# Performance work log

Measured on AMD Instinct MI355X. Metric: run time of the kernel, lower is better.

The kernel has to match this reference:

```python
import jax, jax.numpy as jnp
import numpy as np

EPS = 1e-12

def _l2norm(x):
    # F.normalize(p=2, dim=-1) semantics: x / max(||x||, eps)
    n = jnp.sqrt(jnp.sum(x * x, axis=-1, keepdims=True))
    return x / jnp.maximum(n, EPS)

def _split_heads(x, h):
    b, l, d = x.shape
    return x.reshape(b, l, h, d // h).transpose(0, 2, 1, 3)  # (B,H,L,dh)

def _join_heads(x):
    b, h, l, dh = x.shape
    return x.transpose(0, 2, 1, 3).reshape(b, l, h * dh)

def setup_inputs() -> dict:
    key = jax.random.key(0)
    B, L, D = 4, 4096, 1024
    ks = jax.random.split(key, 12)
    s = 1.0 / np.sqrt(D)
    inp = {
        "queries": jax.random.normal(ks[0], (B, L, D), jnp.float32),
        "values": jax.random.normal(ks[1], (B, L, D), jnp.float32),
        "keys": jax.random.normal(ks[2], (B, L, D), jnp.float32),
        "key_attention_mask": jnp.ones((B, L), jnp.float32),
        "Wq": jax.random.uniform(ks[3], (D, D), jnp.float32, -s, s),
        "bq": jax.random.uniform(ks[4], (D,), jnp.float32, -s, s),
        "Wk": jax.random.uniform(ks[5], (D, D), jnp.float32, -s, s),
        "bk": jax.random.uniform(ks[6], (D,), jnp.float32, -s, s),
        "Wv": jax.random.uniform(ks[7], (D, D), jnp.float32, -s, s),
        "bv": jax.random.uniform(ks[8], (D,), jnp.float32, -s, s),
        "Wo": jax.random.uniform(ks[9], (D, D), jnp.float32, -s, s),
        "bo": jax.random.uniform(ks[10], (D,), jnp.float32, -s, s),
    }
    return inp

def reference(queries, values, keys, key_attention_mask, Wq, bq, Wk, bk, Wv, bv, Wo, bo):
    nhead = 16
    L2 = keys.shape[1]
    qp = jnp.einsum('bld,ed->ble', queries, Wq) + bq
    kp = jnp.einsum('bld,ed->ble', keys, Wk) + bk
    vp = jnp.einsum('bld,ed->ble', values, Wv) + bv
    Q = _split_heads(qp, nhead)   # (B,H,L1,dh)
    K = _split_heads(kp, nhead)   # (B,H,L2,dh)
    V = _split_heads(vp, nhead)   # (B,H,L2,dh)
    V_minus = jnp.minimum(V, 0.0)
    V_plus = jnp.maximum(V, 0.0)
    Q = jax.nn.sigmoid(Q)
    scaled_K = jax.nn.sigmoid(K) / L2
    # AmplitudeEmbedding: L2-normalize feature maps along feature dim
    Q = _l2norm(Q)
    scaled_K = _l2norm(scaled_K)
    kv_plus = jnp.einsum('bhld,bhlc,bl->bhdc', scaled_K, V_plus, key_attention_mask)
    heads_plus = _l2norm(jnp.einsum('bhld,bhdc->bhlc', Q, kv_plus))
    kv_minus = jnp.einsum('bhld,bhlc,bl->bhdc', scaled_K, V_minus, key_attention_mask)
    heads_minus = _l2norm(jnp.einsum('bhld,bhdc->bhlc', Q, kv_minus))
    out = _join_heads(heads_plus + heads_minus)  # (B,L1,D)
    return jnp.einsum('blc,dc->bld', out, Wo) + bo
```

## Files before the change

### kernel.cpp

```cpp
#include <hip/hip_runtime.h>
#include <stdint.h>

#define B_  4
#define L_  4096
#define D_  1024
#define H_  16
#define DH  64
#define M_  (B_*L_)

typedef _Float16 f16;
typedef __attribute__((ext_vector_type(8))) _Float16 f16x8;
typedef __attribute__((ext_vector_type(4))) _Float16 f16x4;
typedef __attribute__((ext_vector_type(4))) float    f32x4;

__device__ __forceinline__ void cp16(const void* g, void* l) {
  __builtin_amdgcn_global_load_lds(
      (const __attribute__((address_space(1))) void*)g,
      (__attribute__((address_space(3))) void*)l,
      16, 0, 0);
}

__global__ __launch_bounds__(256) void k_cvt_f16(const float* __restrict__ x,
                                                 f16* __restrict__ y, int n8) {
  int i = blockIdx.x * 256 + threadIdx.x;
  if (i >= n8) return;
  const float4* xv = (const float4*)x;
  float4 a = xv[2*i], b = xv[2*i+1];
  f16x8 o;
  o[0]=(f16)a.x; o[1]=(f16)a.y; o[2]=(f16)a.z; o[3]=(f16)a.w;
  o[4]=(f16)b.x; o[5]=(f16)b.y; o[6]=(f16)b.z; o[7]=(f16)b.w;
  ((f16x8*)y)[i] = o;
}

__global__ __launch_bounds__(256) void k_split_w(const float* __restrict__ x,
                                                 f16* __restrict__ hi,
                                                 f16* __restrict__ lo, int n4) {
  int i = blockIdx.x * 256 + threadIdx.x;
  if (i >= n4) return;
  float4 a = ((const float4*)x)[i];
  f16 h0=(f16)a.x, h1=(f16)a.y, h2=(f16)a.z, h3=(f16)a.w;
  f16x4 hv = {h0, h1, h2, h3};
  f16x4 lv = {(f16)(a.x-(float)h0), (f16)(a.y-(float)h1),
              (f16)(a.z-(float)h2), (f16)(a.w-(float)h3)};
  ((f16x4*)hi)[i] = hv;
  ((f16x4*)lo)[i] = lv;
}

__global__ __launch_bounds__(256) void k_gemm_hi(
    const f16* __restrict__ A, const f16* __restrict__ Bh,
    const float* __restrict__ bias, const float* __restrict__ mask,
    float* __restrict__ Cf, f16* __restrict__ Ch, int mode,
    int M, int N, int K) {
  __shared__ __align__(16) f16 sA[128*32];
  __shared__ __align__(16) f16 sB[128*32];
  const int t = threadIdx.x;
  const int nbn = N >> 7;
  const int bm = (blockIdx.x / nbn) << 7;
  const int bn = (blockIdx.x % nbn) << 7;
  const int lane = t & 63, wave = t >> 6;
  const int wm = (wave & 1) << 6, wn = (wave >> 1) << 6;
  const int rowA = t >> 2;
  const int cc   = (t & 3) << 3;

  const f16* Ag  = A  + (size_t)(bm + rowA) * K + cc;
  const f16* Ag2 = Ag + (size_t)64 * K;
  const f16* Bg  = Bh + (size_t)(bn + rowA) * K + cc;
  const f16* Bg2 = Bg + (size_t)64 * K;
  f16* lA  = &sA[t * 8];  f16* lA2 = &sA[(t + 256) * 8];
  f16* lB  = &sB[t * 8];  f16* lB2 = &sB[(t + 256) * 8];

  f32x4 acc[4][4] = {};
  const int fm = lane & 15;
  const int fk = (lane >> 4) << 3;

  for (int k0 = 0; k0 < K; k0 += 32) {
    __syncthreads();
    cp16(Ag + k0, lA);  cp16(Ag2 + k0, lA2);
    cp16(Bg + k0, lB);  cp16(Bg2 + k0, lB2);
    __syncthreads();
    f16x8 af[4], bf[4];
#pragma unroll
    for (int i = 0; i < 4; ++i) {
      af[i] = *(const f16x8*)&sA[(wm + i*16 + fm) * 32 + fk];
      bf[i] = *(const f16x8*)&sB[(wn + i*16 + fm) * 32 + fk];
    }
#pragma unroll
    for (int i = 0; i < 4; ++i)
#pragma unroll
      for (int j = 0; j < 4; ++j)
        acc[i][j] = __builtin_amdgcn_mfma_f32_16x16x32_f16(af[i], bf[j], acc[i][j], 0, 0, 0);
  }
  const int cr   = (lane >> 4) << 2;
  const int ccol = lane & 15;
  if (mode == 0) {
#pragma unroll
    for (int j = 0; j < 4; ++j) {
      int gn = bn + wn + j*16 + ccol;
      float bv = bias[gn];
#pragma unroll
      for (int i = 0; i < 4; ++i) {
        float* Cp = Cf + (size_t)(bm + wm + i*16 + cr) * N + gn;
#pragma unroll
        for (int r = 0; r < 4; ++r) Cp[(size_t)r * N] = acc[i][j][r] + bv;
      }
    }
  } else {
    float bvj[4];
#pragma unroll
    for (int j = 0; j < 4; ++j) bvj[j] = bias[bn + wn + j*16 + ccol];
#pragma unroll
    for (int i = 0; i < 4; ++i)
#pragma unroll
      for (int r = 0; r < 4; ++r) {
        int gm = bm + wm + i*16 + cr + r;
        float s[4], ss = 0.f;
#pragma unroll
        for (int j = 0; j < 4; ++j) {
          float v = acc[i][j][r] + bvj[j];
          s[j] = 1.0f / (1.0f + __expf(-v));
          ss += s[j] * s[j];
        }
        ss += __shfl_xor(ss, 1, 64);
        ss += __shfl_xor(ss, 2, 64);
        ss += __shfl_xor(ss, 4, 64);
        ss += __shfl_xor(ss, 8, 64);
        float sc = 1.0f / fmaxf(sqrtf(ss), 1e-12f);
        if (mask) sc *= mask[gm];
#pragma unroll
        for (int j = 0; j < 4; ++j)
          Ch[(size_t)gm * N + bn + wn + j*16 + ccol] = (f16)(s[j] * sc);
      }
  }
}

__global__ __launch_bounds__(256) void k_gemm_ws(
    const f16* __restrict__ A, const f16* __restrict__ Bhi,
    const f16* __restrict__ Blo, const float* __restrict__ bias,
    float* __restrict__ Cf, f16* __restrict__ Ch, int M, int N, int K) {
  __shared__ __align__(16) f16 sA [128*32];
  __shared__ __align__(16) f16 sBh[128*32];
  __shared__ __align__(16) f16 sBl[128*32];
  const int t = threadIdx.x;
  const int nbn = N >> 7;
  const int bm = (blockIdx.x / nbn) << 7;
  const int bn = (blockIdx.x % nbn) << 7;
  const int lane = t & 63, wave = t >> 6;
  const int wm = (wave & 1) << 6, wn = (wave >> 1) << 6;
  const int rowA = t >> 2;
  const int cc   = (t & 3) << 3;

  const f16* Ag   = A   + (size_t)(bm + rowA) * K + cc;
  const f16* Ag2  = Ag  + (size_t)64 * K;
  const f16* Bgh  = Bhi + (size_t)(bn + rowA) * K + cc;
  const f16* Bgh2 = Bgh + (size_t)64 * K;
  const f16* Bgl  = Blo + (size_t)(bn + rowA) * K + cc;
  const f16* Bgl2 = Bgl + (size_t)64 * K;

  f16* lA   = &sA [t * 8];  f16* lA2  = &sA [(t + 256) * 8];
  f16* lBh  = &sBh[t * 8];  f16* lBh2 = &sBh[(t + 256) * 8];
  f16* lBl  = &sBl[t * 8];  f16* lBl2 = &sBl[(t + 256) * 8];

  f32x4 acc[4][4] = {};
  const int fm = lane & 15;
  const int fk = (lane >> 4) << 3;

  for (int k0 = 0; k0 < K; k0 += 32) {
    __syncthreads();
    cp16(Ag  + k0, lA );  cp16(Ag2  + k0, lA2 );
    cp16(Bgh + k0, lBh);  cp16(Bgh2 + k0, lBh2);
    cp16(Bgl + k0, lBl);  cp16(Bgl2 + k0, lBl2);
    __syncthreads();
    f16x8 af[4], bh[4], bl[4];
#pragma unroll
    for (int i = 0; i < 4; ++i) {
      af[i] = *(const f16x8*)&sA [(wm + i*16 + fm) * 32 + fk];
      bh[i] = *(const f16x8*)&sBh[(wn + i*16 + fm) * 32 + fk];
      bl[i] = *(const f16x8*)&sBl[(wn + i*16 + fm) * 32 + fk];
    }
#pragma unroll
    for (int i = 0; i < 4; ++i)
#pragma unroll
      for (int j = 0; j < 4; ++j) {
        acc[i][j] = __builtin_amdgcn_mfma_f32_16x16x32_f16(af[i], bh[j], acc[i][j], 0, 0, 0);
        acc[i][j] = __builtin_amdgcn_mfma_f32_16x16x32_f16(af[i], bl[j], acc[i][j], 0, 0, 0);
      }
  }
  const int cr   = (lane >> 4) << 2;
  const int ccol = lane & 15;
#pragma unroll
  for (int j = 0; j < 4; ++j) {
    int gn = bn + wn + j*16 + ccol;
    float bv = bias[gn];
#pragma unroll
    for (int i = 0; i < 4; ++i) {
      size_t gm = (size_t)(bm + wm + i*16 + cr);
      if (Ch) {
#pragma unroll
        for (int r = 0; r < 4; ++r)
          Ch[(gm + r) * N + gn] = (f16)(acc[i][j][r] + bv);
      } else {
        float* Cp = Cf + gm * N + gn;
#pragma unroll
        for (int r = 0; r < 4; ++r) Cp[(size_t)r * N] = acc[i][j][r] + bv;
      }
    }
  }
}

#define SKT 72
__global__ __launch_bounds__(256) void k_kv_mfma(const f16* __restrict__ Kh,
                                                 const f16* __restrict__ Vh,
                                                 float* __restrict__ part) {
  __shared__ __align__(16) f16 sKt[64 * SKT];
  __shared__ __align__(16) f16 sVt[128 * SKT];
  int head = blockIdx.x >> 3, chunk = blockIdx.x & 7;
  int b = head >> 4, h = head & 15;
  int t = threadIdx.x, lane = t & 63, wave = t >> 6;
  int lp = t & 31, g8 = (t >> 5) << 3;
  size_t rowbase = (size_t)b * L_ + (size_t)chunk * 512;
  const f16* Kb = Kh + rowbase * D_ + h * DH;
  const f16* Vb = Vh + rowbase * D_ + h * DH;

  const int fm = lane & 15, fk = (lane >> 4) << 3;
  const int wm2 = (wave & 1) * 2;
  const int wn4 = (wave >> 1) * 4;
  f32x4 acc[2][4] = {};

  for (int l0 = 0; l0 < 512; l0 += 64) {
    __syncthreads();
    {
      const f16* r0 = Kb + (size_t)(l0 + 2*lp) * D_ + g8;
      f16x8 a0 = *(const f16x8*)r0;
      f16x8 a1 = *(const f16x8*)(r0 + D_);
#pragma unroll
      for (int j = 0; j < 8; ++j) {
        union { f16 h2[2]; uint32_t u; } pk;
        pk.h2[0] = a0[j]; pk.h2[1] = a1[j];
        *(uint32_t*)&sKt[(g8 + j) * SKT + 2*lp] = pk.u;
      }
      const f16* v0p = Vb + (size_t)(l0 + 2*lp) * D_ + g8;
      f16x8 b0 = *(const f16x8*)v0p;
      f16x8 b1 = *(const f16x8*)(v0p + D_);
#pragma unroll
      for (int j = 0; j < 8; ++j) {
        float x0 = (float)b0[j], x1 = (float)b1[j];
        union { f16 h2[2]; uint32_t u; } pp, pm;
        pp.h2[0] = (f16)fmaxf(x0, 0.f); pp.h2[1] = (f16)fmaxf(x1, 0.f);
        pm.h2[0] = (f16)fminf(x0, 0.f); pm.h2[1] = (f16)fminf(x1, 0.f);
        *(uint32_t*)&sVt[(g8 + j) * SKT + 2*lp]        = pp.u;
        *(uint32_t*)&sVt[(64 + g8 + j) * SKT + 2*lp]   = pm.u;
      }
    }
    __syncthreads();
#pragma unroll
    for (int ks = 0; ks < 2; ++ks) {
      f16x8 af[2], bf[4];
#pragma unroll
      for (int i = 0; i < 2; ++i)
        af[i] = *(const f16x8*)&sKt[((wm2+i)*16 + fm) * SKT + ks*32 + fk];
#pragma unroll
      for (int j = 0; j < 4; ++j)
        bf[j] = *(const f16x8*)&sVt[((wn4+j)*16 + fm) * SKT + ks*32 + fk];
#pragma unroll
      for (int i = 0; i < 2; ++i)
#pragma unroll
        for (int j = 0; j < 4; ++j)
          acc[i][j] = __builtin_amdgcn_mfma_f32_16x16x32_f16(af[i], bf[j], acc[i][j], 0, 0, 0);
    }
  }
  const int cr = (lane >> 4) << 2, ccol = lane & 15;
  float* pb = part + (size_t)(head * 8 + chunk) * 8192;
#pragma unroll
  for (int i = 0; i < 2; ++i)
#pragma unroll
    for (int j = 0; j < 4; ++j) {
      int d = (wm2 + i) * 16 + cr;
      int c2 = (wn4 + j) * 16 + ccol;
#pragma unroll
      for (int r = 0; r < 4; ++r)
        pb[(d + r) * 128 + c2] = acc[i][j][r];
    }
}

__global__ __launch_bounds__(256) void k_kv_reduce(const float* __restrict__ part,
                                                   float* __restrict__ kv) {
  int i = blockIdx.x * 256 + threadIdx.x;
  int head = i >> 13, dc = i & 8191;
  float s = 0.f;
#pragma unroll
  for (int c = 0; c < 8; ++c) s += part[(size_t)(head * 8 + c) * 8192 + dc];
  kv[i] = s;
}

__global__ __launch_bounds__(256) void k_kv_cvt(const float* __restrict__ kvb,
                                                f16* __restrict__ kvh) {
  int head = blockIdx.x, t = threadIdx.x;
  int c = t >> 1, half = t & 1;
  const float* src = kvb + (size_t)head * 8192 + half * 32 * 128 + c;
  f16* dst = kvh + (size_t)head * 8192 + c * 64 + half * 32;
  f16 buf[32];
#pragma unroll
  for (int kk = 0; kk < 32; ++kk) buf[kk] = (f16)src[kk * 128];
#pragma unroll
  for (int q = 0; q < 4; ++q) ((f16x8*)dst)[q] = *(const f16x8*)&buf[q * 8];
}

#define SH 72
__global__ __launch_bounds__(256) void k_heads_mfma(const f16* __restrict__ Qh,
                                                    const f16* __restrict__ kvh,
                                                    f16* __restrict__ O) {
  __shared__ __align__(16) f16 sQ [128 * SH];
  __shared__ __align__(16) f16 sKV[128 * SH];
  int bi = blockIdx.x;
  int head = bi >> 5, mt = bi & 31;
  int b = head >> 4, h = head & 15;
  int t = threadIdx.x, lane = t & 63, wave = t >> 6;
  size_t qbase = ((size_t)(b * L_ + mt * 128)) * D_ + h * DH;
  const f16* kvp = kvh + (size_t)head * 8192;
#pragma unroll
  for (int p = 0; p < 4; ++p) {
    int c = p * 256 + t;
    int row = c >> 3, off = (c & 7) * 8;
    f16x8 q = *(const f16x8*)(Qh + qbase + (size_t)row * D_ + off);
    *(f16x8*)&sQ[row * SH + off] = q;
    f16x8 kv8 = *(const f16x8*)(kvp + row * 64 + off);
    *(f16x8*)&sKV[row * SH + off] = kv8;
  }
  __syncthreads();

  const int fm = lane & 15, fk = (lane >> 4) << 3;
  const int wm = wave * 32;
  f32x4 acc[2][8] = {};
#pragma unroll
  for (int ks = 0; ks < 2; ++ks) {
    f16x8 a0 = *(const f16x8*)&sQ[(wm + fm) * SH + ks * 32 + fk];
    f16x8 a1 = *(const f16x8*)&sQ[(wm + 16 + fm) * SH + ks * 32 + fk];
#pragma unroll
    for (int j = 0; j < 8; ++j) {
      f16x8 bj = *(const f16x8*)&sKV[(j * 16 + fm) * SH + ks * 32 + fk];
      acc[0][j] = __builtin_amdgcn_mfma_f32_16x16x32_f16(a0, bj, acc[0][j], 0, 0, 0);
      acc[1][j] = __builtin_amdgcn_mfma_f32_16x16x32_f16(a1, bj, acc[1][j], 0, 0, 0);
    }
  }
  const int cr = (lane >> 4) << 2, ccol = lane & 15;
#pragma unroll
  for (int i = 0; i < 2; ++i)
#pragma unroll
    for (int r = 0; r < 4; ++r) {
      int row = wm + i * 16 + cr + r;
      float sp = 0.f, sm = 0.f;
#pragma unroll
      for (int j = 0; j < 4; ++j) {
        sp += acc[i][j][r] * acc[i][j][r];
        sm += acc[i][j + 4][r] * acc[i][j + 4][r];
      }
      sp += __shfl_xor(sp, 1, 64); sm += __shfl_xor(sm, 1, 64);
      sp += __shfl_xor(sp, 2, 64); sm += __shfl_xor(sm, 2, 64);
      sp += __shfl_xor(sp, 4, 64); sm += __shfl_xor(sm, 4, 64);
      sp += __shfl_xor(sp, 8, 64); sm += __shfl_xor(sm, 8, 64);
      float rp = 1.0f / fmaxf(sqrtf(sp), 1e-12f);
      float rm = 1.0f / fmaxf(sqrtf(sm), 1e-12f);
#pragma unroll
      for (int j = 0; j < 4; ++j) {
        float o = acc[i][j][r] * rp + acc[i][j + 4][r] * rm;
        O[qbase + (size_t)row * D_ + j * 16 + ccol] = (f16)o;
      }
    }
}

extern "C" void kernel_launch(void* const* d_in, const int* in_sizes, int n_in,
                              void* d_out, int out_size, void* d_ws, size_t ws_size,
                              hipStream_t stream) {
  const float* queries = (const float*)d_in[0];
  const float* values  = (const float*)d_in[1];
  const float* keys    = (const float*)d_in[2];
  const float* mask    = (const float*)d_in[3];
  const float* Wq = (const float*)d_in[4];  const float* bq = (const float*)d_in[5];
  const float* Wk = (const float*)d_in[6];  const float* bk = (const float*)d_in[7];
  const float* Wv = (const float*)d_in[8];  const float* bv = (const float*)d_in[9];
  const float* Wo = (const float*)d_in[10]; const float* bo = (const float*)d_in[11];
  float* out = (float*)d_out;

  const size_t MB = 1024ull * 1024ull;
  const size_t NEED = 160 * MB;
  if (ws_size < NEED) return;

  char* ws = (char*)d_ws;
  const size_t DD = (size_t)D_ * D_;
  f16*   WH   = (f16*)(ws);
  f16*   WL   = (f16*)(ws + 8 * MB);
  f16*   Ah   = (f16*)(ws + 12 * MB);
  f16*   Qh   = (f16*)(ws + 44 * MB);
  float* kvb  = (float*)(ws + 76 * MB);
  f16*   kvh  = (f16*)(ws + 78 * MB);
  float* part = (float*)(ws + 80 * MB);
  f16*   kp   = (f16*)(ws + 96 * MB);
  f16*   vp   = (f16*)(ws + 128 * MB);

  const int DD8 = (int)(DD / 8);
  const int DD4 = (int)(DD / 4);
  k_cvt_f16<<<DD8 / 256, 256, 0, stream>>>(Wq, WH + 0 * DD, DD8);
  k_cvt_f16<<<DD8 / 256, 256, 0, stream>>>(Wk, WH + 1 * DD, DD8);
  k_split_w<<<DD4 / 256, 256, 0, stream>>>(Wv, WH + 2 * DD, WL + 0 * DD, DD4);
  k_split_w<<<DD4 / 256, 256, 0, stream>>>(Wo, WH + 3 * DD, WL + 1 * DD, DD4);

  const int n8 = M_ * D_ / 8;
  const int gGemm = (M_ / 128) * (D_ / 128);

  k_cvt_f16<<<n8 / 256, 256, 0, stream>>>(queries, Ah, n8);
  k_gemm_hi<<<gGemm, 256, 0, stream>>>(Ah, WH + 0 * DD, bq, nullptr, nullptr, Qh, 1, M_, D_, D_);
  k_cvt_f16<<<n8 / 256, 256, 0, stream>>>(keys, Ah, n8);
  k_gemm_hi<<<gGemm, 256, 0, stream>>>(Ah, WH + 1 * DD, bk, mask, nullptr, kp, 1, M_, D_, D_);
  k_cvt_f16<<<n8 / 256, 256, 0, stream>>>(values, Ah, n8);
  k_gemm_ws<<<gGemm, 256, 0, stream>>>(Ah, WH + 2 * DD, WL + 0 * DD, bv, nullptr, vp, M_, D_, D_);

  k_kv_mfma<<<64 * 8, 256, 0, stream>>>(kp, vp, part);
  k_kv_reduce<<<64 * 8192 / 256, 256, 0, stream>>>(part, kvb);
  k_kv_cvt<<<64, 256, 0, stream>>>(kvb, kvh);
  k_heads_mfma<<<64 * 32, 256, 0, stream>>>(Qh, kvh, Ah);

  k_gemm_ws<<<gGemm, 256, 0, stream>>>(Ah, WH + 3 * DD, WL + 1 * DD, bo, out, nullptr, M_, D_, D_);
}
```

Baseline: 615.0 us.

## Replace GEMMs with 256x256 double-buffered 8-wave kernel and interleaved hi/lo weights

Replaces the two 128x128 GEMM kernels with a single 512-thread kernel that uses 256x256 tiles, 64-wide K steps, XOR-swizzled LDS and double-buffered async global-to-LDS loads. MFMA phases are interleaved with loads and use setprio and barriers. The hi/lo split weights are interleaved row-wise into one 2N matrix, so the split-precision GEMMs become plain GEMMs over N=2048 whose paired column tiles are summed in the epilogue. Blocks are also remapped across the 8 XCDs. The aim is more data reuse and better MFMA utilization, at the cost of large LDS usage, register pressure and fragile hand scheduling.

```diff
diff --git a/kernel.cpp b/kernel.cpp
--- a/kernel.cpp
+++ b/kernel.cpp
@@ -19,6 +19,21 @@
       (__attribute__((address_space(3))) void*)l,
       16, 0, 0);
 }
+
+#define MFMA(a,b,c) __builtin_amdgcn_mfma_f32_16x16x32_f16(a,b,c,0,0,0)
+
+#define PH_IN do { __builtin_amdgcn_s_barrier(); \
+  asm volatile("s_waitcnt lgkmcnt(0)" ::: "memory"); \
+  __builtin_amdgcn_sched_barrier(0); \
+  __builtin_amdgcn_s_setprio(1); } while (0)
+#define PH_OUT do { __builtin_amdgcn_s_setprio(0); \
+  __builtin_amdgcn_sched_barrier(0); \
+  asm volatile("" ::: "memory"); \
+  __builtin_amdgcn_s_barrier(); } while (0)
+#define PH_OUT_VM(nimm) do { __builtin_amdgcn_s_setprio(0); \
+  __builtin_amdgcn_sched_barrier(0); \
+  asm volatile("s_waitcnt vmcnt(" #nimm ")" ::: "memory"); \
+  __builtin_amdgcn_s_barrier(); } while (0)
 
 __global__ __launch_bounds__(256) void k_cvt_f16(const float* __restrict__ x,
                                                  f16* __restrict__ y, int n8) {
@@ -33,86 +48,197 @@
 }
 
 __global__ __launch_bounds__(256) void k_split_w(const float* __restrict__ x,
-                                                 f16* __restrict__ hi,
-                                                 f16* __restrict__ lo, int n4) {
+                                                 f16* __restrict__ cat, int n4) {
   int i = blockIdx.x * 256 + threadIdx.x;
   if (i >= n4) return;
   float4 a = ((const float4*)x)[i];
+  int n  = i >> 8;
+  int k4 = i & 255;
   f16 h0=(f16)a.x, h1=(f16)a.y, h2=(f16)a.z, h3=(f16)a.w;
   f16x4 hv = {h0, h1, h2, h3};
   f16x4 lv = {(f16)(a.x-(float)h0), (f16)(a.y-(float)h1),
               (f16)(a.z-(float)h2), (f16)(a.w-(float)h3)};
-  ((f16x4*)hi)[i] = hv;
-  ((f16x4*)lo)[i] = lv;
-}
-
-__global__ __launch_bounds__(256) void k_gemm_hi(
-    const f16* __restrict__ A, const f16* __restrict__ Bh,
+  size_t rh = (size_t)((n >> 4) * 32 + (n & 15));
+  ((f16x4*)cat)[rh * 256 + k4]        = hv;
+  ((f16x4*)cat)[(rh + 16) * 256 + k4] = lv;
+}
+
+__global__ __launch_bounds__(512, 2) void k_gemm8(
+    const f16* __restrict__ A, const f16* __restrict__ Bw,
     const float* __restrict__ bias, const float* __restrict__ mask,
     float* __restrict__ Cf, f16* __restrict__ Ch, int mode,
     int M, int N, int K) {
-  __shared__ __align__(16) f16 sA[128*32];
-  __shared__ __align__(16) f16 sB[128*32];
+  __shared__ __align__(16) char sA[65536];
+  __shared__ __align__(16) char sB[65536];
   const int t = threadIdx.x;
-  const int nbn = N >> 7;
-  const int bm = (blockIdx.x / nbn) << 7;
-  const int bn = (blockIdx.x % nbn) << 7;
+  const int nbn = N >> 8;
+  int bid = blockIdx.x;
+  {
+    int cpx = (int)gridDim.x >> 3;
+    bid = (bid & 7) * cpx + (bid >> 3);
+  }
+  const int bm = (bid / nbn) << 8;
+  const int bn = (bid % nbn) << 8;
   const int lane = t & 63, wave = t >> 6;
-  const int wm = (wave & 1) << 6, wn = (wave >> 1) << 6;
-  const int rowA = t >> 2;
-  const int cc   = (t & 3) << 3;
-
-  const f16* Ag  = A  + (size_t)(bm + rowA) * K + cc;
-  const f16* Ag2 = Ag + (size_t)64 * K;
-  const f16* Bg  = Bh + (size_t)(bn + rowA) * K + cc;
-  const f16* Bg2 = Bg + (size_t)64 * K;
-  f16* lA  = &sA[t * 8];  f16* lA2 = &sA[(t + 256) * 8];
-  f16* lB  = &sB[t * 8];  f16* lB2 = &sB[(t + 256) * 8];
-
-  f32x4 acc[4][4] = {};
-  const int fm = lane & 15;
-  const int fk = (lane >> 4) << 3;
-
-  for (int k0 = 0; k0 < K; k0 += 32) {
-    __syncthreads();
-    cp16(Ag + k0, lA);  cp16(Ag2 + k0, lA2);
-    cp16(Bg + k0, lB);  cp16(Bg2 + k0, lB2);
-    __syncthreads();
-    f16x8 af[4], bf[4];
-#pragma unroll
-    for (int i = 0; i < 4; ++i) {
-      af[i] = *(const f16x8*)&sA[(wm + i*16 + fm) * 32 + fk];
-      bf[i] = *(const f16x8*)&sB[(wn + i*16 + fm) * 32 + fk];
-    }
-#pragma unroll
-    for (int i = 0; i < 4; ++i)
-#pragma unroll
-      for (int j = 0; j < 4; ++j)
-        acc[i][j] = __builtin_amdgcn_mfma_f32_16x16x32_f16(af[i], bf[j], acc[i][j], 0, 0, 0);
-  }
-  const int cr   = (lane >> 4) << 2;
-  const int ccol = lane & 15;
-  if (mode == 0) {
-#pragma unroll
-    for (int j = 0; j < 4; ++j) {
-      int gn = bn + wn + j*16 + ccol;
-      float bv = bias[gn];
-#pragma unroll
-      for (int i = 0; i < 4; ++i) {
-        float* Cp = Cf + (size_t)(bm + wm + i*16 + cr) * N + gn;
-#pragma unroll
-        for (int r = 0; r < 4; ++r) Cp[(size_t)r * N] = acc[i][j][r] + bv;
-      }
-    }
-  } else {
+  const int wm = wave >> 2;
+  const int wn = wave & 3;
+  const int fm = lane & 15, fkb = lane >> 4;
+
+  auto SA_ = [&](int T, int buf, int half) {
+#pragma unroll
+    for (int q = 0; q < 2; ++q) {
+      int li = (q << 9) + t;
+      int row = li >> 3, cb = li & 7;
+      const f16* g = A + (size_t)(bm + (half << 7) + row) * K
+                       + (T << 6) + ((cb ^ (row & 7)) << 3);
+      cp16(g, sA + buf * 32768 + half * 16384 + li * 16);
+    }
+  };
+  auto SB_ = [&](int T, int buf, int half) {
+#pragma unroll
+    for (int q = 0; q < 2; ++q) {
+      int li = (q << 9) + t;
+      int row = li >> 3, cb = li & 7;
+      const f16* g = Bw + (size_t)(bn + (half << 7) + row) * K
+                        + (T << 6) + ((cb ^ (row & 7)) << 3);
+      cp16(g, sB + buf * 32768 + half * 16384 + li * 16);
+    }
+  };
+  auto LDA = [&](int buf, int i, int ks) -> f16x8 {
+    int row = (i << 4) + fm;
+    int blk = ((ks << 2) + fkb) ^ (row & 7);
+    return *(const f16x8*)(sA + buf * 32768 + (wm << 14) + (row << 7) + (blk << 4));
+  };
+  auto LDB = [&](int buf, int j, int ks) -> f16x8 {
+    int row = ((wn & 1) << 6) + (j << 4) + fm;
+    int blk = ((ks << 2) + fkb) ^ (row & 7);
+    return *(const f16x8*)(sB + buf * 32768 + ((wn >> 1) << 14) + (row << 7) + (blk << 4));
+  };
+
+  f32x4 acc[8][4] = {};
+
+  SA_(0, 0, 0); SA_(0, 0, 1);
+  SB_(0, 0, 0); SB_(0, 0, 1);
+  SB_(1, 1, 0); SB_(1, 1, 1);
+  asm volatile("s_waitcnt vmcnt(4)" ::: "memory");
+  __builtin_amdgcn_s_barrier();
+
+  const int NI = K >> 7;
+  for (int it = 0; it < NI; ++it) {
+    const bool nl = (it != NI - 1);
+    const int t2 = 2 * it + 2, t3 = 2 * it + 3;
+    f16x8 aL[4][2], aH[4][2], bA[2][2], bB[2][2];
+
+#pragma unroll
+    for (int i = 0; i < 4; ++i) { aL[i][0] = LDA(0,i,0); aL[i][1] = LDA(0,i,1); }
+#pragma unroll
+    for (int j = 0; j < 2; ++j) { bA[j][0] = LDB(0,j,0); bA[j][1] = LDB(0,j,1); }
+    SA_(2*it+1, 1, 0);
+    PH_IN;
+#pragma unroll
+    for (int i = 0; i < 4; ++i)
+#pragma unroll
+      for (int j = 0; j < 2; ++j) {
+        acc[i][j] = MFMA(aL[i][0], bA[j][0], acc[i][j]);
+        acc[i][j] = MFMA(aL[i][1], bA[j][1], acc[i][j]);
+      }
+    PH_OUT;
+#pragma unroll
+    for (int j = 0; j < 2; ++j) { bB[j][0] = LDB(0,j+2,0); bB[j][1] = LDB(0,j+2,1); }
+    SA_(2*it+1, 1, 1);
+    PH_IN;
+#pragma unroll
+    for (int i = 0; i < 4; ++i)
+#pragma unroll
+      for (int j = 0; j < 2; ++j) {
+        acc[i][j+2] = MFMA(aL[i][0], bB[j][0], acc[i][j+2]);
+        acc[i][j+2] = MFMA(aL[i][1], bB[j][1], acc[i][j+2]);
+      }
+    PH_OUT;
+#pragma unroll
+    for (int i = 0; i < 4; ++i) { aH[i][0] = LDA(0,i+4,0); aH[i][1] = LDA(0,i+4,1); }
+    if (nl) SB_(t2, 0, 0);
+    PH_IN;
+#pragma unroll
+    for (int i = 0; i < 4; ++i)
+#pragma unroll
+      for (int j = 0; j < 2; ++j) {
+        acc[i+4][j] = MFMA(aH[i][0], bA[j][0], acc[i+4][j]);
+        acc[i+4][j] = MFMA(aH[i][1], bA[j][1], acc[i+4][j]);
+      }
+    PH_OUT;
+    if (nl) SB_(t2, 0, 1);
+    PH_IN;
+#pragma unroll
+    for (int i = 0; i < 4; ++i)
+#pragma unroll
+      for (int j = 0; j < 2; ++j) {
+        acc[i+4][j+2] = MFMA(aH[i][0], bB[j][0], acc[i+4][j+2]);
+        acc[i+4][j+2] = MFMA(aH[i][1], bB[j][1], acc[i+4][j+2]);
+      }
+    if (nl) PH_OUT_VM(4); else PH_OUT_VM(0);
+#pragma unroll
+    for (int i = 0; i < 4; ++i) { aL[i][0] = LDA(1,i,0); aL[i][1] = LDA(1,i,1); }
+#pragma unroll
+    for (int j = 0; j < 2; ++j) { bA[j][0] = LDB(1,j,0); bA[j][1] = LDB(1,j,1); }
+    if (nl) SA_(t2, 0, 0);
+    PH_IN;
+#pragma unroll
+    for (int i = 0; i < 4; ++i)
+#pragma unroll
+      for (int j = 0; j < 2; ++j) {
+        acc[i][j] = MFMA(aL[i][0], bA[j][0], acc[i][j]);
+        acc[i][j] = MFMA(aL[i][1], bA[j][1], acc[i][j]);
+      }
+    PH_OUT;
+#pragma unroll
+    for (int j = 0; j < 2; ++j) { bB[j][0] = LDB(1,j+2,0); bB[j][1] = LDB(1,j+2,1); }
+    if (nl) SA_(t2, 0, 1);
+    PH_IN;
+#pragma unroll
+    for (int i = 0; i < 4; ++i)
+#pragma unroll
+      for (int j = 0; j < 2; ++j) {
+        acc[i][j+2] = MFMA(aL[i][0], bB[j][0], acc[i][j+2]);
+        acc[i][j+2] = MFMA(aL[i][1], bB[j][1], acc[i][j+2]);
+      }
+    PH_OUT;
+#pragma unroll
+    for (int i = 0; i < 4; ++i) { aH[i][0] = LDA(1,i+4,0); aH[i][1] = LDA(1,i+4,1); }
+    if (nl) SB_(t3, 1, 0);
+    PH_IN;
+#pragma unroll
+    for (int i = 0; i < 4; ++i)
+#pragma unroll
+      for (int j = 0; j < 2; ++j) {
+        acc[i+4][j] = MFMA(aH[i][0], bA[j][0], acc[i+4][j]);
+        acc[i+4][j] = MFMA(aH[i][1], bA[j][1], acc[i+4][j]);
+      }
+    PH_OUT;
+    if (nl) SB_(t3, 1, 1);
+    PH_IN;
+#pragma unroll
+    for (int i = 0; i < 4; ++i)
+#pragma unroll
+      for (int j = 0; j < 2; ++j) {
+        acc[i+4][j+2] = MFMA(aH[i][0], bB[j][0], acc[i+4][j+2]);
+        acc[i+4][j+2] = MFMA(aH[i][1], bB[j][1], acc[i+4][j+2]);
+      }
+    PH_OUT_VM(4);
+  }
+
+  const int cr = (lane >> 4) << 2, ccol = lane & 15;
+  const int rowbase = bm + wm * 128;
+  if (mode == 1) {
+    const int No = N;
     float bvj[4];
 #pragma unroll
-    for (int j = 0; j < 4; ++j) bvj[j] = bias[bn + wn + j*16 + ccol];
-#pragma unroll
-    for (int i = 0; i < 4; ++i)
+    for (int j = 0; j < 4; ++j) bvj[j] = bias[bn + wn*64 + j*16 + ccol];
+#pragma unroll
+    for (int i = 0; i < 8; ++i)
 #pragma unroll
       for (int r = 0; r < 4; ++r) {
-        int gm = bm + wm + i*16 + cr + r;
+        int gm = rowbase + i*16 + cr + r;
         float s[4], ss = 0.f;
 #pragma unroll
         for (int j = 0; j < 4; ++j) {
@@ -128,81 +254,24 @@
         if (mask) sc *= mask[gm];
 #pragma unroll
         for (int j = 0; j < 4; ++j)
-          Ch[(size_t)gm * N + bn + wn + j*16 + ccol] = (f16)(s[j] * sc);
-      }
-  }
-}
-
-__global__ __launch_bounds__(256) void k_gemm_ws(
-    const f16* __restrict__ A, const f16* __restrict__ Bhi,
-    const f16* __restrict__ Blo, const float* __restrict__ bias,
-    float* __restrict__ Cf, f16* __restrict__ Ch, int M, int N, int K) {
-  __shared__ __align__(16) f16 sA [128*32];
-  __shared__ __align__(16) f16 sBh[128*32];
-  __shared__ __align__(16) f16 sBl[128*32];
-  const int t = threadIdx.x;
-  const int nbn = N >> 7;
-  const int bm = (blockIdx.x / nbn) << 7;
-  const int bn = (blockIdx.x % nbn) << 7;
-  const int lane = t & 63, wave = t >> 6;
-  const int wm = (wave & 1) << 6, wn = (wave >> 1) << 6;
-  const int rowA = t >> 2;
-  const int cc   = (t & 3) << 3;
-
-  const f16* Ag   = A   + (size_t)(bm + rowA) * K + cc;
-  const f16* Ag2  = Ag  + (size_t)64 * K;
-  const f16* Bgh  = Bhi + (size_t)(bn + rowA) * K + cc;
-  const f16* Bgh2 = Bgh + (size_t)64 * K;
-  const f16* Bgl  = Blo + (size_t)(bn + rowA) * K + cc;
-  const f16* Bgl2 = Bgl + (size_t)64 * K;
-
-  f16* lA   = &sA [t * 8];  f16* lA2  = &sA [(t + 256) * 8];
-  f16* lBh  = &sBh[t * 8];  f16* lBh2 = &sBh[(t + 256) * 8];
-  f16* lBl  = &sBl[t * 8];  f16* lBl2 = &sBl[(t + 256) * 8];
-
-  f32x4 acc[4][4] = {};
-  const int fm = lane & 15;
-  const int fk = (lane >> 4) << 3;
-
-  for (int k0 = 0; k0 < K; k0 += 32) {
-    __syncthreads();
-    cp16(Ag  + k0, lA );  cp16(Ag2  + k0, lA2 );
-    cp16(Bgh + k0, lBh);  cp16(Bgh2 + k0, lBh2);
-    cp16(Bgl + k0, lBl);  cp16(Bgl2 + k0, lBl2);
-    __syncthreads();
-    f16x8 af[4], bh[4], bl[4];
-#pragma unroll
-    for (int i = 0; i < 4; ++i) {
-      af[i] = *(const f16x8*)&sA [(wm + i*16 + fm) * 32 + fk];
-      bh[i] = *(const f16x8*)&sBh[(wn + i*16 + fm) * 32 + fk];
-      bl[i] = *(const f16x8*)&sBl[(wn + i*16 + fm) * 32 + fk];
-    }
-#pragma unroll
-    for (int i = 0; i < 4; ++i)
-#pragma unroll
-      for (int j = 0; j < 4; ++j) {
-        acc[i][j] = __builtin_amdgcn_mfma_f32_16x16x32_f16(af[i], bh[j], acc[i][j], 0, 0, 0);
-        acc[i][j] = __builtin_amdgcn_mfma_f32_16x16x32_f16(af[i], bl[j], acc[i][j], 0, 0, 0);
-      }
-  }
-  const int cr   = (lane >> 4) << 2;
-  const int ccol = lane & 15;
-#pragma unroll
-  for (int j = 0; j < 4; ++j) {
-    int gn = bn + wn + j*16 + ccol;
-    float bv = bias[gn];
-#pragma unroll
-    for (int i = 0; i < 4; ++i) {
-      size_t gm = (size_t)(bm + wm + i*16 + cr);
-      if (Ch) {
-#pragma unroll
-        for (int r = 0; r < 4; ++r)
-          Ch[(gm + r) * N + gn] = (f16)(acc[i][j][r] + bv);
-      } else {
-        float* Cp = Cf + gm * N + gn;
-#pragma unroll
-        for (int r = 0; r < 4; ++r) Cp[(size_t)r * N] = acc[i][j][r] + bv;
-      }
+          Ch[(size_t)gm * No + bn + wn*64 + j*16 + ccol] = (f16)(s[j] * sc);
+      }
+  } else {
+    const int No = N >> 1;
+#pragma unroll
+    for (int j2 = 0; j2 < 2; ++j2) {
+      int colp = bn + wn*64 + (2*j2)*16;
+      int oc = ((colp >> 5) << 4) + ccol;
+      float bv = bias[oc];
+#pragma unroll
+      for (int i = 0; i < 8; ++i)
+#pragma unroll
+        for (int r = 0; r < 4; ++r) {
+          int gm = rowbase + i*16 + cr + r;
+          float v = acc[i][2*j2][r] + acc[i][2*j2+1][r] + bv;
+          if (mode == 2) Ch[(size_t)gm * No + oc] = (f16)v;
+          else           Cf[(size_t)gm * No + oc] = v;
+        }
     }
   }
 }
@@ -265,7 +334,7 @@
       for (int i = 0; i < 2; ++i)
 #pragma unroll
         for (int j = 0; j < 4; ++j)
-          acc[i][j] = __builtin_amdgcn_mfma_f32_16x16x32_f16(af[i], bf[j], acc[i][j], 0, 0, 0);
+          acc[i][j] = MFMA(af[i], bf[j], acc[i][j]);
     }
   }
   const int cr = (lane >> 4) << 2, ccol = lane & 15;
@@ -338,8 +407,8 @@
 #pragma unroll
     for (int j = 0; j < 8; ++j) {
       f16x8 bj = *(const f16x8*)&sKV[(j * 16 + fm) * SH + ks * 32 + fk];
-      acc[0][j] = __builtin_amdgcn_mfma_f32_16x16x32_f16(a0, bj, acc[0][j], 0, 0, 0);
-      acc[1][j] = __builtin_amdgcn_mfma_f32_16x16x32_f16(a1, bj, acc[1][j], 0, 0, 0);
+      acc[0][j] = MFMA(a0, bj, acc[0][j]);
+      acc[1][j] = MFMA(a1, bj, acc[1][j]);
     }
   }
   const int cr = (lane >> 4) << 2, ccol = lane & 15;
@@ -387,8 +456,10 @@
 
   char* ws = (char*)d_ws;
   const size_t DD = (size_t)D_ * D_;
-  f16*   WH   = (f16*)(ws);
-  f16*   WL   = (f16*)(ws + 8 * MB);
+  f16*   Wqh  = (f16*)(ws);
+  f16*   Wkh  = (f16*)(ws + 2 * MB);
+  f16*   Wcv  = (f16*)(ws + 4 * MB);
+  f16*   Wco  = (f16*)(ws + 8 * MB);
   f16*   Ah   = (f16*)(ws + 12 * MB);
   f16*   Qh   = (f16*)(ws + 44 * MB);
   float* kvb  = (float*)(ws + 76 * MB);
@@ -399,25 +470,26 @@
 
   const int DD8 = (int)(DD / 8);
   const int DD4 = (int)(DD / 4);
-  k_cvt_f16<<<DD8 / 256, 256, 0, stream>>>(Wq, WH + 0 * DD, DD8);
-  k_cvt_f16<<<DD8 / 256, 256, 0, stream>>>(Wk, WH + 1 * DD, DD8);
-  k_split_w<<<DD4 / 256, 256, 0, stream>>>(Wv, WH + 2 * DD, WL + 0 * DD, DD4);
-  k_split_w<<<DD4 / 256, 256, 0, stream>>>(Wo, WH + 3 * DD, WL + 1 * DD, DD4);
+  k_cvt_f16<<<DD8 / 256, 256, 0, stream>>>(Wq, Wqh, DD8);
+  k_cvt_f16<<<DD8 / 256, 256, 0, stream>>>(Wk, Wkh, DD8);
+  k_split_w<<<DD4 / 256, 256, 0, stream>>>(Wv, Wcv, DD4);
+  k_split_w<<<DD4 / 256, 256, 0, stream>>>(Wo, Wco, DD4);
 
   const int n8 = M_ * D_ / 8;
-  const int gGemm = (M_ / 128) * (D_ / 128);
+  const int g1 = (M_ / 256) * (1024 / 256);
+  const int g2 = (M_ / 256) * (2048 / 256);
 
   k_cvt_f16<<<n8 / 256, 256, 0, stream>>>(queries, Ah, n8);
-  k_gemm_hi<<<gGemm, 256, 0, stream>>>(Ah, WH + 0 * DD, bq, nullptr, nullptr, Qh, 1, M_, D_, D_);
+  k_gemm8<<<g1, 512, 0, stream>>>(Ah, Wqh, bq, nullptr, nullptr, Qh, 1, M_, 1024, 1024);
   k_cvt_f16<<<n8 / 256, 256, 0, stream>>>(keys, Ah, n8);
-  k_gemm_hi<<<gGemm, 256, 0, stream>>>(Ah, WH + 1 * DD, bk, mask, nullptr, kp, 1, M_, D_, D_);
+  k_gemm8<<<g1, 512, 0, stream>>>(Ah, Wkh, bk, mask, nullptr, kp, 1, M_, 1024, 1024);
   k_cvt_f16<<<n8 / 256, 256, 0, stream>>>(values, Ah, n8);
-  k_gemm_ws<<<gGemm, 256, 0, stream>>>(Ah, WH + 2 * DD, WL + 0 * DD, bv, nullptr, vp, M_, D_, D_);
+  k_gemm8<<<g2, 512, 0, stream>>>(Ah, Wcv, bv, nullptr, nullptr, vp, 2, M_, 2048, 1024);
 
   k_kv_mfma<<<64 * 8, 256, 0, stream>>>(kp, vp, part);
   k_kv_reduce<<<64 * 8192 / 256, 256, 0, stream>>>(part, kvb);
   k_kv_cvt<<<64, 256, 0, stream>>>(kvb, kvh);
   k_heads_mfma<<<64 * 32, 256, 0, stream>>>(Qh, kvh, Ah);
 
-  k_gemm_ws<<<gGemm, 256, 0, stream>>>(Ah, WH + 3 * DD, WL + 1 * DD, bo, out, nullptr, M_, D_, D_);
-}
+  k_gemm8<<<g2, 512, 0, stream>>>(Ah, Wco, bo, nullptr, out, nullptr, 3, M_, 2048, 1024);
+}
```

Measured after the change: 554.6 us. 1.11x faster.
